# Kernel tuning notes

Hardware: AMD Instinct MI355X
Metric: run time of the kernel (lower is better)

Reference implementation:

```python
import jax, jax.numpy as jnp
import numpy as np

N = 100000   # nodes
E = 1200000  # directed edges (avg degree 12)
D = 64       # in_feats
C = 40       # n_classes
K = 16       # propagation steps
ALPHA = 0.05


def setup_inputs() -> dict:
    key = jax.random.key(0)
    k1, k2, k3, k4 = jax.random.split(key, 4)
    feat = jax.random.normal(k1, (N, D), jnp.float32)
    # xavier_uniform for fc.weight [C, D]
    limit = np.sqrt(6.0 / (D + C)).astype(np.float32)
    W = jax.random.uniform(k2, (C, D), jnp.float32, -limit, limit)
    b = jnp.zeros((C,), jnp.float32)
    src = jax.random.randint(k3, (E,), 0, N, dtype=jnp.int32)
    dst = jax.random.randint(k4, (E,), 0, N, dtype=jnp.int32)
    return {"feat": feat, "W": W, "b": b, "src": src, "dst": dst}


def reference(feat, W, b, src, dst):
    # --- getNormAugAdj: A_hat = D^{-1/2} (A + I) D^{-1/2} ---
    loops = jnp.arange(N, dtype=src.dtype)
    row = jnp.concatenate([dst, loops])  # output node of each edge
    col = jnp.concatenate([src, loops])  # input  node of each edge
    ones = jnp.ones(row.shape, feat.dtype)
    deg = jax.ops.segment_sum(ones, row, num_segments=N)  # >= 1 (self-loops)
    dinv = jax.lax.rsqrt(deg)
    w = dinv[row] * dinv[col]  # per-edge normalized weight

    def spmm(x):  # x: [N, D] -> A_hat @ x
        return jax.ops.segment_sum(w[:, None] * x[col], row, num_segments=N)

    feat_ori = feat

    # SSGC loop (faithful to the original, including h /= K inside the loop)
    def step(carry, _):
        x, h = carry
        x = spmm(x)
        h = (h + (1.0 - ALPHA) * x + ALPHA * feat_ori) / K
        return (x, h), None

    (_, h), _ = jax.lax.scan(step, (feat, jnp.zeros_like(feat)), None, length=K)

    # fc(h)
    return h @ W.T + b
```

## Files before the change

### kernel.cpp

```cpp
#include <hip/hip_runtime.h>
#include <hip/hip_fp16.h>

#define NN 100000
#define EE 1200000
#define DD 64
#define CC 40
#define KK 16
#define BSZ 196
#define NBK 512
#define TCAP 3072
#define EPB 4096
#define ABLK ((EE + EPB - 1) / EPB)

struct __align__(8) ERec { int c; float w; };

__global__ __launch_bounds__(512) void curinit_kernel(int* __restrict__ cursor) {
    int b = threadIdx.x;
    if (b < NBK) cursor[b] = b * TCAP;
}

__global__ __launch_bounds__(256) void sortA_kernel(const int* __restrict__ src,
                                                    const int* __restrict__ dst,
                                                    int* __restrict__ cursor,
                                                    int2* __restrict__ tmp) {
    __shared__ int2 stg[EPB];
    __shared__ int hist[NBK], loff[NBK], lcur[NBK], gbase[NBK];
    int t = threadIdx.x;
    long e0 = (long)blockIdx.x * EPB;
    int n = (int)((EE - e0 < EPB) ? (EE - e0) : EPB);
    for (int j = t; j < NBK; j += 256) hist[j] = 0;
    __syncthreads();
    int d[16], sx[16];
#pragma unroll
    for (int j = 0; j < 16; ++j) {
        int i = t + j * 256;
        if (i < n) {
            d[j] = dst[e0 + i];
            sx[j] = src[e0 + i];
            atomicAdd(&hist[d[j] / BSZ], 1);
        } else d[j] = -1;
    }
    __syncthreads();
    int c0 = hist[2 * t], c1 = hist[2 * t + 1];
    int s2 = c0 + c1;
    __syncthreads();
    loff[t] = s2;
    __syncthreads();
    for (int off = 1; off < 256; off <<= 1) {
        int u = (t >= off) ? loff[t - off] : 0;
        __syncthreads();
        loff[t] += u;
        __syncthreads();
    }
    int excl = loff[t] - s2;
    __syncthreads();
    loff[2 * t] = excl;          loff[2 * t + 1] = excl + c0;
    lcur[2 * t] = excl;          lcur[2 * t + 1] = excl + c0;
    gbase[2 * t]     = atomicAdd(&cursor[2 * t], c0);
    gbase[2 * t + 1] = atomicAdd(&cursor[2 * t + 1], c1);
    __syncthreads();
#pragma unroll
    for (int j = 0; j < 16; ++j) {
        if (d[j] >= 0) {
            int b = d[j] / BSZ;
            int p = atomicAdd(&lcur[b], 1);
            stg[p] = make_int2(d[j], sx[j]);
        }
    }
    __syncthreads();
    for (int i = t; i < n; i += 256) {
        int2 r = stg[i];
        int b = r.x / BSZ;
        int pos = gbase[b] + (i - loff[b]);
        if (pos < (b + 1) * TCAP) tmp[pos] = r;
    }
}

__global__ __launch_bounds__(512) void bscan_kernel(const int* __restrict__ cursor,
                                                    int* __restrict__ bbase,
                                                    int* __restrict__ row_ptr) {
    __shared__ int sm[512];
    int t = threadIdx.x;
    int v = (t < NBK) ? (cursor[t] - t * TCAP) : 0;
    sm[t] = v;
    __syncthreads();
    for (int off = 1; off < 512; off <<= 1) {
        int u = (t >= off) ? sm[t - off] : 0;
        __syncthreads();
        sm[t] += u;
        __syncthreads();
    }
    if (t < NBK) bbase[t] = sm[t] - v;
    if (t == 511) row_ptr[NN] = sm[511];
}

__global__ __launch_bounds__(256) void sortB_kernel(const int2* __restrict__ tmp,
                                                    const int* __restrict__ cursor,
                                                    const int* __restrict__ bbase,
                                                    float* __restrict__ dinv,
                                                    int* __restrict__ row_ptr,
                                                    int2* __restrict__ er2) {
    __shared__ int2 se[TCAP];
    __shared__ int2 so[TCAP];
    __shared__ int hist[256], lcur[256];
    int b = blockIdx.x;
    int n0 = b * BSZ;
    if (n0 >= NN) return;
    int n1 = n0 + BSZ; if (n1 > NN) n1 = NN;
    int nb = n1 - n0;
    int t = threadIdx.x;
    int cnt = cursor[b] - b * TCAP;
    int base = bbase[b];
    hist[t] = 0;
    __syncthreads();
    for (int i = t; i < cnt; i += 256) {
        int2 r = tmp[b * TCAP + i];
        se[i] = r;
        atomicAdd(&hist[r.x - n0], 1);
    }
    __syncthreads();
    if (t < nb) dinv[n0 + t] = rsqrtf((float)(hist[t] + 1));
    int v = hist[t];
    lcur[t] = v;
    __syncthreads();
    for (int off = 1; off < 256; off <<= 1) {
        int u = (t >= off) ? lcur[t - off] : 0;
        __syncthreads();
        lcur[t] += u;
        __syncthreads();
    }
    int excl = lcur[t] - v;
    __syncthreads();
    lcur[t] = excl;
    if (t < nb) row_ptr[n0 + t] = base + excl;
    __syncthreads();
    for (int i = t; i < cnt; i += 256) {
        int2 r = se[i];
        int ln = r.x - n0;
        int pos = atomicAdd(&lcur[ln], 1);
        so[pos] = make_int2(r.y, r.x);
    }
    __syncthreads();
    for (int i = t; i < cnt; i += 256) er2[base + i] = so[i];
}

__global__ __launch_bounds__(256) void wfill_kernel(const int2* __restrict__ er2,
                                                    const float* __restrict__ dinv,
                                                    int2* __restrict__ er) {
    int i = blockIdx.x * 256 + threadIdx.x;
    if (i >= EE) return;
    int2 r = er2[i];
    float w = dinv[r.y] * dinv[r.x];
    er[i] = make_int2(r.x, __float_as_int(w));
}

__global__ __launch_bounds__(256) void cvt_kernel(const float2* __restrict__ feat2,
                                                  __half2* __restrict__ xh) {
    int i = blockIdx.x * 256 + threadIdx.x;
    if (i < NN * 32) {
        float2 f = feat2[i];
        xh[i] = __floats2half2_rn(f.x, f.y);
    }
}

__global__ __launch_bounds__(256) void spmm_step(
    const float4* __restrict__ x, float4* __restrict__ x_out,
    float4* __restrict__ h4, const float4* __restrict__ feat4,
    const int* __restrict__ row_ptr, const ERec* __restrict__ er,
    const float* __restrict__ dinv, int mode) {
    int g = (blockIdx.x * 256 + threadIdx.x) >> 3;
    int li = threadIdx.x & 7;
    int beg = row_ptr[g], end = row_ptr[g + 1];
    float di = dinv[g];
    float w0 = di * di;
    int base = g * 8 + li;
    float4 sv = x[base];
    float a0, a1, a2, a3, a4, a5, a6, a7;
    {
        const __half2* hp = (const __half2*)&sv;
        float2 f0 = __half22float2(hp[0]), f1 = __half22float2(hp[1]);
        float2 f2 = __half22float2(hp[2]), f3 = __half22float2(hp[3]);
        a0 = w0 * f0.x; a1 = w0 * f0.y; a2 = w0 * f1.x; a3 = w0 * f1.y;
        a4 = w0 * f2.x; a5 = w0 * f2.y; a6 = w0 * f3.x; a7 = w0 * f3.y;
    }
#define ACC8(R, V)                                                          \
    {                                                                       \
        const __half2* hp = (const __half2*)&(V);                           \
        float2 f0 = __half22float2(hp[0]), f1 = __half22float2(hp[1]);      \
        float2 f2 = __half22float2(hp[2]), f3 = __half22float2(hp[3]);      \
        a0 = fmaf((R).w, f0.x, a0); a1 = fmaf((R).w, f0.y, a1);             \
        a2 = fmaf((R).w, f1.x, a2); a3 = fmaf((R).w, f1.y, a3);             \
        a4 = fmaf((R).w, f2.x, a4); a5 = fmaf((R).w, f2.y, a5);             \
        a6 = fmaf((R).w, f3.x, a6); a7 = fmaf((R).w, f3.y, a7);             \
    }
    int e = beg;
    int e4 = beg + ((end - beg) & ~3);
    for (; e < e4; e += 4) {
        ERec r0 = er[e], r1 = er[e + 1], r2 = er[e + 2], r3 = er[e + 3];
        float4 v0 = x[r0.c * 8 + li];
        float4 v1 = x[r1.c * 8 + li];
        float4 v2 = x[r2.c * 8 + li];
        float4 v3 = x[r3.c * 8 + li];
        ACC8(r0, v0); ACC8(r1, v1); ACC8(r2, v2); ACC8(r3, v3);
    }
    for (; e < end; ++e) {
        ERec r = er[e];
        float4 v = x[r.c * 8 + li];
        ACC8(r, v);
    }
#undef ACC8
    if (mode != 3) {
        float4 ov;
        __half2* op = (__half2*)&ov;
        op[0] = __floats2half2_rn(a0, a1);
        op[1] = __floats2half2_rn(a2, a3);
        op[2] = __floats2half2_rn(a4, a5);
        op[3] = __floats2half2_rn(a6, a7);
        x_out[base] = ov;
    }
    if (mode) {
        int hb = g * 16 + li * 2;
        float4 h0, h1;
        if (mode == 1) {
            h0.x = 0.95f * a0 * (1.0f / 16.0f); h0.y = 0.95f * a1 * (1.0f / 16.0f);
            h0.z = 0.95f * a2 * (1.0f / 16.0f); h0.w = 0.95f * a3 * (1.0f / 16.0f);
            h1.x = 0.95f * a4 * (1.0f / 16.0f); h1.y = 0.95f * a5 * (1.0f / 16.0f);
            h1.z = 0.95f * a6 * (1.0f / 16.0f); h1.w = 0.95f * a7 * (1.0f / 16.0f);
        } else {
            h0 = h4[hb]; h1 = h4[hb + 1];
            h0.x = (h0.x + 0.95f * a0) * (1.0f / 16.0f);
            h0.y = (h0.y + 0.95f * a1) * (1.0f / 16.0f);
            h0.z = (h0.z + 0.95f * a2) * (1.0f / 16.0f);
            h0.w = (h0.w + 0.95f * a3) * (1.0f / 16.0f);
            h1.x = (h1.x + 0.95f * a4) * (1.0f / 16.0f);
            h1.y = (h1.y + 0.95f * a5) * (1.0f / 16.0f);
            h1.z = (h1.z + 0.95f * a6) * (1.0f / 16.0f);
            h1.w = (h1.w + 0.95f * a7) * (1.0f / 16.0f);
        }
        if (mode == 3) {
            const float FC = 0.05f / 15.0f;
            float4 f0 = feat4[hb], f1 = feat4[hb + 1];
            h0.x = fmaf(FC, f0.x, h0.x); h0.y = fmaf(FC, f0.y, h0.y);
            h0.z = fmaf(FC, f0.z, h0.z); h0.w = fmaf(FC, f0.w, h0.w);
            h1.x = fmaf(FC, f1.x, h1.x); h1.y = fmaf(FC, f1.y, h1.y);
            h1.z = fmaf(FC, f1.z, h1.z); h1.w = fmaf(FC, f1.w, h1.w);
        }
        h4[hb] = h0; h4[hb + 1] = h1;
    }
}

__global__ __launch_bounds__(256) void fc_kernel(const float* __restrict__ h,
                                                 const float* __restrict__ W,
                                                 const float* __restrict__ b,
                                                 float* __restrict__ out) {
    __shared__ float Ws[CC * 65];
    __shared__ float bs[CC];
    for (int j = threadIdx.x; j < CC * DD; j += 256) {
        int c = j >> 6, d = j & 63;
        Ws[c * 65 + d] = W[j];
    }
    if (threadIdx.x < CC) bs[threadIdx.x] = b[threadIdx.x];
    __syncthreads();
    int idx = blockIdx.x * 256 + threadIdx.x;
    if (idx >= NN * CC) return;
    int i = idx / CC, c = idx - i * CC;
    const float4* h4 = (const float4*)(h + (long)i * DD);
    const float* wr = Ws + c * 65;
    float acc = bs[c];
#pragma unroll
    for (int d2 = 0; d2 < 16; ++d2) {
        float4 a = h4[d2];
        acc = fmaf(a.x, wr[d2 * 4 + 0], acc);
        acc = fmaf(a.y, wr[d2 * 4 + 1], acc);
        acc = fmaf(a.z, wr[d2 * 4 + 2], acc);
        acc = fmaf(a.w, wr[d2 * 4 + 3], acc);
    }
    out[idx] = acc;
}

extern "C" void kernel_launch(void* const* d_in, const int* in_sizes, int n_in,
                              void* d_out, int out_size, void* d_ws, size_t ws_size,
                              hipStream_t stream) {
    const float* feat = (const float*)d_in[0];
    const float* W    = (const float*)d_in[1];
    const float* b    = (const float*)d_in[2];
    const int*   src  = (const int*)d_in[3];
    const int*   dst  = (const int*)d_in[4];
    float* out = (float*)d_out;

    char* p = (char*)d_ws;
    auto alloc = [&](size_t bytes) {
        char* r = p;
        p += (bytes + 255) & ~(size_t)255;
        return r;
    };
    float*   dinv    = (float*)alloc((size_t)NN * sizeof(float));
    int*     row_ptr = (int*)alloc((size_t)(NN + 1) * sizeof(int));
    int*     cursor  = (int*)alloc((size_t)NBK * sizeof(int));
    int*     bbase   = (int*)alloc((size_t)NBK * sizeof(int));
    int2*    tmp     = (int2*)alloc((size_t)NBK * TCAP * sizeof(int2));
    int2*    er2     = (int2*)alloc((size_t)EE * sizeof(int2));
    int2*    er      = (int2*)alloc((size_t)EE * sizeof(int2));
    float4*  xh0     = (float4*)alloc((size_t)NN * 8 * sizeof(float4));
    float4*  xh1     = (float4*)alloc((size_t)NN * 8 * sizeof(float4));
    float*   h       = (float*)alloc((size_t)NN * DD * sizeof(float));

    curinit_kernel<<<1, 512, 0, stream>>>(cursor);
    sortA_kernel<<<ABLK, 256, 0, stream>>>(src, dst, cursor, tmp);
    bscan_kernel<<<1, 512, 0, stream>>>(cursor, bbase, row_ptr);
    sortB_kernel<<<NBK, 256, 0, stream>>>(tmp, cursor, bbase, dinv, row_ptr, er2);
    wfill_kernel<<<(EE + 255) / 256, 256, 0, stream>>>(er2, dinv, er);
    cvt_kernel<<<(NN * 32 + 255) / 256, 256, 0, stream>>>((const float2*)feat,
                                                          (__half2*)xh0);

    const float4* xs = xh0;
    float4* xd = xh1;
    for (int j = 0; j < KK; ++j) {
        int mode = (j < 10) ? 0 : ((j == 10) ? 1 : ((j == KK - 1) ? 3 : 2));
        spmm_step<<<3125, 256, 0, stream>>>(xs, xd, (float4*)h, (const float4*)feat,
                                            row_ptr, (const ERec*)er, dinv, mode);
        const float4* t = xd;
        xd = (xd == xh0) ? xh1 : xh0;
        xs = t;
    }
    fc_kernel<<<(NN * CC + 255) / 256, 256, 0, stream>>>(h, W, b, out);
}
```

Measured before the change: 626.0 us.

## Project features to class space before propagation and fuse FC into last step

Uses linearity to apply the W projection to feat first, so all 16 SpMM steps propagate 40-wide half vectors instead of 64-wide ones. Thread mapping changes to 5 lanes per node with 12 nodes per wavefront, and a planar layout splits 32 channels from the last 8. The final step adds bias and the alpha*feat term (now projected) and writes the output directly, which removes the separate fc kernel and the h read. It cuts gather bandwidth per step. In exchange it leaves 4 lanes per wave idle, uses uneven index math, and adds a register-heavy projection kernel with 40 accumulators.

```diff
diff --git a/kernel.cpp b/kernel.cpp
--- a/kernel.cpp
+++ b/kernel.cpp
@@ -11,6 +11,7 @@
 #define TCAP 3072
 #define EPB 4096
 #define ABLK ((EE + EPB - 1) / EPB)
+#define PL1 (NN * 4)
 
 struct __align__(8) ERec { int c; float w; };
 
@@ -154,26 +155,62 @@
     er[i] = make_int2(r.x, __float_as_int(w));
 }
 
-__global__ __launch_bounds__(256) void cvt_kernel(const float2* __restrict__ feat2,
-                                                  __half2* __restrict__ xh) {
-    int i = blockIdx.x * 256 + threadIdx.x;
-    if (i < NN * 32) {
-        float2 f = feat2[i];
-        xh[i] = __floats2half2_rn(f.x, f.y);
+__global__ __launch_bounds__(256) void proj_kernel(const float4* __restrict__ feat4,
+                                                   const float* __restrict__ W,
+                                                   float4* __restrict__ y0) {
+    __shared__ float4 Wld[CC * 16];
+    int t = threadIdx.x;
+    for (int j = t; j < CC * 16; j += 256) Wld[j] = ((const float4*)W)[j];
+    __syncthreads();
+    int i = blockIdx.x * 256 + t;
+    if (i >= NN) return;
+    float acc[CC];
+#pragma unroll
+    for (int c = 0; c < CC; ++c) acc[c] = 0.f;
+    const float4* f = feat4 + (size_t)i * 16;
+#pragma unroll
+    for (int d2 = 0; d2 < 16; ++d2) {
+        float4 fv = f[d2];
+#pragma unroll
+        for (int c = 0; c < CC; ++c) {
+            float4 wv = Wld[c * 16 + d2];
+            acc[c] = fmaf(fv.x, wv.x, acc[c]);
+            acc[c] = fmaf(fv.y, wv.y, acc[c]);
+            acc[c] = fmaf(fv.z, wv.z, acc[c]);
+            acc[c] = fmaf(fv.w, wv.w, acc[c]);
+        }
+    }
+#pragma unroll
+    for (int q = 0; q < 5; ++q) {
+        float4 ov;
+        __half2* op = (__half2*)&ov;
+        op[0] = __floats2half2_rn(acc[q * 8 + 0], acc[q * 8 + 1]);
+        op[1] = __floats2half2_rn(acc[q * 8 + 2], acc[q * 8 + 3]);
+        op[2] = __floats2half2_rn(acc[q * 8 + 4], acc[q * 8 + 5]);
+        op[3] = __floats2half2_rn(acc[q * 8 + 6], acc[q * 8 + 7]);
+        y0[(q < 4) ? ((size_t)i * 4 + q) : (size_t)(PL1 + i)] = ov;
     }
 }
 
 __global__ __launch_bounds__(256) void spmm_step(
     const float4* __restrict__ x, float4* __restrict__ x_out,
-    float4* __restrict__ h4, const float4* __restrict__ feat4,
+    const float4* __restrict__ y0, float4* __restrict__ h4,
+    float* __restrict__ outp, const float* __restrict__ bias,
     const int* __restrict__ row_ptr, const ERec* __restrict__ er,
     const float* __restrict__ dinv, int mode) {
-    int g = (blockIdx.x * 256 + threadIdx.x) >> 3;
-    int li = threadIdx.x & 7;
+    int tid = blockIdx.x * 256 + threadIdx.x;
+    int wid = tid >> 6;
+    int lane = tid & 63;
+    int nw = lane / 5;
+    int li = lane - nw * 5;
+    int g = wid * 12 + nw;
+    if (nw >= 12 || g >= NN) return;
     int beg = row_ptr[g], end = row_ptr[g + 1];
     float di = dinv[g];
     float w0 = di * di;
-    int base = g * 8 + li;
+    int m = (li < 4) ? 4 : 1;
+    int a = (li < 4) ? li : PL1;
+    int base = g * m + a;
     float4 sv = x[base];
     float a0, a1, a2, a3, a4, a5, a6, a7;
     {
@@ -197,15 +234,15 @@
     int e4 = beg + ((end - beg) & ~3);
     for (; e < e4; e += 4) {
         ERec r0 = er[e], r1 = er[e + 1], r2 = er[e + 2], r3 = er[e + 3];
-        float4 v0 = x[r0.c * 8 + li];
-        float4 v1 = x[r1.c * 8 + li];
-        float4 v2 = x[r2.c * 8 + li];
-        float4 v3 = x[r3.c * 8 + li];
+        float4 v0 = x[r0.c * m + a];
+        float4 v1 = x[r1.c * m + a];
+        float4 v2 = x[r2.c * m + a];
+        float4 v3 = x[r3.c * m + a];
         ACC8(r0, v0); ACC8(r1, v1); ACC8(r2, v2); ACC8(r3, v3);
     }
     for (; e < end; ++e) {
         ERec r = er[e];
-        float4 v = x[r.c * 8 + li];
+        float4 v = x[r.c * m + a];
         ACC8(r, v);
     }
 #undef ACC8
@@ -219,7 +256,7 @@
         x_out[base] = ov;
     }
     if (mode) {
-        int hb = g * 16 + li * 2;
+        int hb = g * 10 + li * 2;
         float4 h0, h1;
         if (mode == 1) {
             h0.x = 0.95f * a0 * (1.0f / 16.0f); h0.y = 0.95f * a1 * (1.0f / 16.0f);
@@ -239,43 +276,26 @@
         }
         if (mode == 3) {
             const float FC = 0.05f / 15.0f;
-            float4 f0 = feat4[hb], f1 = feat4[hb + 1];
-            h0.x = fmaf(FC, f0.x, h0.x); h0.y = fmaf(FC, f0.y, h0.y);
-            h0.z = fmaf(FC, f0.z, h0.z); h0.w = fmaf(FC, f0.w, h0.w);
-            h1.x = fmaf(FC, f1.x, h1.x); h1.y = fmaf(FC, f1.y, h1.y);
-            h1.z = fmaf(FC, f1.z, h1.z); h1.w = fmaf(FC, f1.w, h1.w);
+            float4 yv = y0[base];
+            const __half2* yp = (const __half2*)&yv;
+            float2 y01 = __half22float2(yp[0]), y23 = __half22float2(yp[1]);
+            float2 y45 = __half22float2(yp[2]), y67 = __half22float2(yp[3]);
+            const float4* b4 = (const float4*)(bias + li * 8);
+            float4 bb0 = b4[0], bb1 = b4[1];
+            h0.x = fmaf(FC, y01.x, h0.x) + bb0.x;
+            h0.y = fmaf(FC, y01.y, h0.y) + bb0.y;
+            h0.z = fmaf(FC, y23.x, h0.z) + bb0.z;
+            h0.w = fmaf(FC, y23.y, h0.w) + bb0.w;
+            h1.x = fmaf(FC, y45.x, h1.x) + bb1.x;
+            h1.y = fmaf(FC, y45.y, h1.y) + bb1.y;
+            h1.z = fmaf(FC, y67.x, h1.z) + bb1.z;
+            h1.w = fmaf(FC, y67.y, h1.w) + bb1.w;
+            float4* op = (float4*)(outp + (size_t)g * CC + li * 8);
+            op[0] = h0; op[1] = h1;
+        } else {
+            h4[hb] = h0; h4[hb + 1] = h1;
         }
-        h4[hb] = h0; h4[hb + 1] = h1;
-    }
-}
-
-__global__ __launch_bounds__(256) void fc_kernel(const float* __restrict__ h,
-                                                 const float* __restrict__ W,
-                                                 const float* __restrict__ b,
-                                                 float* __restrict__ out) {
-    __shared__ float Ws[CC * 65];
-    __shared__ float bs[CC];
-    for (int j = threadIdx.x; j < CC * DD; j += 256) {
-        int c = j >> 6, d = j & 63;
-        Ws[c * 65 + d] = W[j];
-    }
-    if (threadIdx.x < CC) bs[threadIdx.x] = b[threadIdx.x];
-    __syncthreads();
-    int idx = blockIdx.x * 256 + threadIdx.x;
-    if (idx >= NN * CC) return;
-    int i = idx / CC, c = idx - i * CC;
-    const float4* h4 = (const float4*)(h + (long)i * DD);
-    const float* wr = Ws + c * 65;
-    float acc = bs[c];
-#pragma unroll
-    for (int d2 = 0; d2 < 16; ++d2) {
-        float4 a = h4[d2];
-        acc = fmaf(a.x, wr[d2 * 4 + 0], acc);
-        acc = fmaf(a.y, wr[d2 * 4 + 1], acc);
-        acc = fmaf(a.z, wr[d2 * 4 + 2], acc);
-        acc = fmaf(a.w, wr[d2 * 4 + 3], acc);
-    }
-    out[idx] = acc;
+    }
 }
 
 extern "C" void kernel_launch(void* const* d_in, const int* in_sizes, int n_in,
@@ -301,27 +321,26 @@
     int2*    tmp     = (int2*)alloc((size_t)NBK * TCAP * sizeof(int2));
     int2*    er2     = (int2*)alloc((size_t)EE * sizeof(int2));
     int2*    er      = (int2*)alloc((size_t)EE * sizeof(int2));
-    float4*  xh0     = (float4*)alloc((size_t)NN * 8 * sizeof(float4));
-    float4*  xh1     = (float4*)alloc((size_t)NN * 8 * sizeof(float4));
-    float*   h       = (float*)alloc((size_t)NN * DD * sizeof(float));
+    float4*  y0      = (float4*)alloc((size_t)NN * 5 * sizeof(float4));
+    float4*  xa      = (float4*)alloc((size_t)NN * 5 * sizeof(float4));
+    float4*  xb      = (float4*)alloc((size_t)NN * 5 * sizeof(float4));
+    float4*  h       = (float4*)alloc((size_t)NN * 10 * sizeof(float4));
 
     curinit_kernel<<<1, 512, 0, stream>>>(cursor);
     sortA_kernel<<<ABLK, 256, 0, stream>>>(src, dst, cursor, tmp);
     bscan_kernel<<<1, 512, 0, stream>>>(cursor, bbase, row_ptr);
     sortB_kernel<<<NBK, 256, 0, stream>>>(tmp, cursor, bbase, dinv, row_ptr, er2);
     wfill_kernel<<<(EE + 255) / 256, 256, 0, stream>>>(er2, dinv, er);
-    cvt_kernel<<<(NN * 32 + 255) / 256, 256, 0, stream>>>((const float2*)feat,
-                                                          (__half2*)xh0);
-
-    const float4* xs = xh0;
-    float4* xd = xh1;
+    proj_kernel<<<(NN + 255) / 256, 256, 0, stream>>>((const float4*)feat, W, y0);
+
+    const int SPMM_BLOCKS = (8334 + 3) / 4;
+    const float4* xs = y0;
+    float4* xd = xa;
     for (int j = 0; j < KK; ++j) {
         int mode = (j < 10) ? 0 : ((j == 10) ? 1 : ((j == KK - 1) ? 3 : 2));
-        spmm_step<<<3125, 256, 0, stream>>>(xs, xd, (float4*)h, (const float4*)feat,
-                                            row_ptr, (const ERec*)er, dinv, mode);
-        const float4* t = xd;
-        xd = (xd == xh0) ? xh1 : xh0;
-        xs = t;
-    }
-    fc_kernel<<<(NN * CC + 255) / 256, 256, 0, stream>>>(h, W, b, out);
-}
+        spmm_step<<<SPMM_BLOCKS, 256, 0, stream>>>(xs, xd, y0, h, out, b,
+                                                   row_ptr, (const ERec*)er, dinv, mode);
+        xs = xd;
+        xd = (xd == xa) ? xb : xa;
+    }
+}
```

Result: slower. 644.4 us (+2.9%).
